# Kernel tuning notes

Measured on AMD Instinct MI355X. Metric: run time of the kernel, lower is better.

Reference implementation:

```python
import jax, jax.numpy as jnp
import numpy as np

D_MODEL = 1024
NUM_HEADS = 16
HEAD_DIM = D_MODEL // NUM_HEADS
T = 4096


def setup_inputs() -> dict:
    key = jax.random.key(0)
    x = jax.random.normal(key, (T, D_MODEL), dtype=jnp.float32)
    return {"x": x}


def reference(x) -> jnp.ndarray:
    T_, _ = x.shape
    # q = k = v = x reshaped to [heads, T, head_dim]
    qkv = x.reshape(T_, NUM_HEADS, HEAD_DIM).transpose(1, 0, 2)  # [H, T, hd]
    scale = 1.0 / (HEAD_DIM ** 0.5)
    scores = jnp.einsum('htd,hsd->hts', qkv, qkv) * scale  # [H, T, T]
    attn = jax.nn.softmax(scores, axis=-1)
    out = jnp.einsum('hts,hsd->htd', attn, qkv)  # [H, T, hd]
    return out.transpose(1, 0, 2).reshape(T_, D_MODEL)
```

## Files before the change

kernel.cpp:

```cpp
#include <hip/hip_runtime.h>
#include <hip/hip_bf16.h>

#define T_SEQ 4096
#define DMODEL 1024
#define NHEADS 16
#define HDIM 64
#define QBLK 256
#define SBLK 64
#define NTILES (T_SEQ / SBLK)
#define KSPLIT 2
#define TILES_PER_SPLIT (NTILES / KSPLIT)

#define KV_BYTES ((size_t)NHEADS * NTILES * 16384)
#define P_BYTES  ((size_t)KSPLIT * T_SEQ * DMODEL * 4)
#define L_BYTES  ((size_t)KSPLIT * NHEADS * T_SEQ * 4)
#define WS_NEEDED (KV_BYTES + P_BYTES + L_BYTES)

typedef __attribute__((ext_vector_type(8))) __bf16 bf16x8;
typedef __attribute__((ext_vector_type(4))) __bf16 bf16x4;
typedef __attribute__((ext_vector_type(16))) float f32x16;
typedef __attribute__((ext_vector_type(2))) unsigned uint32x2;

#define SWZ(row, col) ((col) ^ (((row) & 7) << 3))

#define QSCALE 0.1803368801111204f

__device__ __forceinline__ unsigned cvt_pk_bf16(float lo, float hi) {
  unsigned r;
  asm("v_cvt_pk_bf16_f32 %0, %1, %2" : "=v"(r) : "v"(lo), "v"(hi));
  return r;
}
__device__ __forceinline__ uint32x2 plswap(unsigned a, unsigned b) {
  return __builtin_amdgcn_permlane32_swap(a, b, false, false);
}
__device__ __forceinline__ float xhalf_max(float v) {
  uint32x2 r = plswap(__float_as_uint(v), __float_as_uint(v));
  return fmaxf(__uint_as_float(r[0]), __uint_as_float(r[1]));
}
__device__ __forceinline__ float xhalf_sum(float v) {
  uint32x2 r = plswap(__float_as_uint(v), __float_as_uint(v));
  return __uint_as_float(r[0]) + __uint_as_float(r[1]);
}
__device__ __forceinline__ void glds16(const void* g, void* l) {
  __builtin_amdgcn_global_load_lds(
      (const __attribute__((address_space(1))) unsigned int*)g,
      (__attribute__((address_space(3))) unsigned int*)l, 16, 0, 0);
}

__global__ __launch_bounds__(256) void prepass_kernel(
    const float* __restrict__ x, unsigned char* __restrict__ kvimg) {
  const int tid = threadIdx.x;
  const int c4 = tid & 15, s4 = tid >> 4;
  const int t = blockIdx.x & (NTILES - 1), h = blockIdx.x >> 6;
  const float* src = x + (size_t)(t * SBLK + s4 * 4) * DMODEL + h * HDIM + c4 * 4;
  float4 r0 = *reinterpret_cast<const float4*>(src);
  float4 r1 = *reinterpret_cast<const float4*>(src + DMODEL);
  float4 r2 = *reinterpret_cast<const float4*>(src + 2 * DMODEL);
  float4 r3 = *reinterpret_cast<const float4*>(src + 3 * DMODEL);
  __bf16 b[4][4];
  b[0][0] = (__bf16)r0.x; b[0][1] = (__bf16)r0.y; b[0][2] = (__bf16)r0.z; b[0][3] = (__bf16)r0.w;
  b[1][0] = (__bf16)r1.x; b[1][1] = (__bf16)r1.y; b[1][2] = (__bf16)r1.z; b[1][3] = (__bf16)r1.w;
  b[2][0] = (__bf16)r2.x; b[2][1] = (__bf16)r2.y; b[2][2] = (__bf16)r2.z; b[2][3] = (__bf16)r2.w;
  b[3][0] = (__bf16)r3.x; b[3][1] = (__bf16)r3.y; b[3][2] = (__bf16)r3.z; b[3][3] = (__bf16)r3.w;
  __bf16* Kimg = (__bf16*)(kvimg + (size_t)blockIdx.x * 16384);
  __bf16* Vimg = Kimg + 4096;
  #pragma unroll
  for (int j = 0; j < 4; j++) {
    const int s = s4 * 4 + j;
    bf16x4 kv; kv[0] = b[j][0]; kv[1] = b[j][1]; kv[2] = b[j][2]; kv[3] = b[j][3];
    *reinterpret_cast<bf16x4*>(&Kimg[s * 64 + SWZ(s, c4 * 4)]) = kv;
  }
  #pragma unroll
  for (int i = 0; i < 4; i++) {
    const int d = c4 * 4 + i;
    bf16x4 vv; vv[0] = b[0][i]; vv[1] = b[1][i]; vv[2] = b[2][i]; vv[3] = b[3][i];
    *reinterpret_cast<bf16x4*>(&Vimg[d * 64 + SWZ(d, s4 * 4)]) = vv;
  }
}

__global__ __launch_bounds__(256, 2) void attn_main_kernel(
    const float* __restrict__ x, const unsigned char* __restrict__ kvimg,
    float* __restrict__ pbuf, float* __restrict__ lbuf) {
  const int tid  = threadIdx.x;
  const int wave = tid >> 6;
  const int lane = tid & 63;
  const int lq   = lane & 31;
  const int hi   = lane >> 5;

  const int qt = blockIdx.x & 15;
  const int h  = blockIdx.x >> 4;
  const int sp = blockIdx.y;

  __shared__ __align__(16) unsigned char kvbytes[2][16384];

  bf16x8 qf[2][4];
  const int qrow0 = qt * QBLK + wave * 64 + lq;
  #pragma unroll
  for (int qs = 0; qs < 2; qs++) {
    const float* qp = x + (size_t)(qrow0 + qs * 32) * DMODEL + h * HDIM;
    #pragma unroll
    for (int ds = 0; ds < 4; ds++) {
      float4 a = *reinterpret_cast<const float4*>(qp + ds * 16 + hi * 8);
      float4 b = *reinterpret_cast<const float4*>(qp + ds * 16 + hi * 8 + 4);
      bf16x8 f;
      f[0] = (__bf16)(QSCALE * a.x); f[1] = (__bf16)(QSCALE * a.y);
      f[2] = (__bf16)(QSCALE * a.z); f[3] = (__bf16)(QSCALE * a.w);
      f[4] = (__bf16)(QSCALE * b.x); f[5] = (__bf16)(QSCALE * b.y);
      f[6] = (__bf16)(QSCALE * b.z); f[7] = (__bf16)(QSCALE * b.w);
      qf[qs][ds] = f;
    }
  }

  f32x16 oacc[2][2];
  float lsum[2];
  #pragma unroll
  for (int qs = 0; qs < 2; qs++) {
    #pragma unroll
    for (int dt = 0; dt < 2; dt++)
      #pragma unroll
      for (int r = 0; r < 16; r++) oacc[qs][dt][r] = 0.f;
    lsum[qs] = 0.f;
  }

  const unsigned char* tbase =
      kvimg + ((size_t)(h * NTILES + sp * TILES_PER_SPLIT) * 16384);

  auto STAGE = [&](int buf, int t) {
    const unsigned char* g = tbase + (size_t)t * 16384;
    #pragma unroll
    for (int i = 0; i < 4; i++)
      glds16(g + i * 4096 + tid * 16, &kvbytes[buf][i * 4096 + tid * 16]);
  };

  STAGE(0, 0);
  __syncthreads();
  int cur = 0;

  for (int t = 0; t < TILES_PER_SPLIT; t++) {
    if (t + 1 < TILES_PER_SPLIT) STAGE(cur ^ 1, t + 1);
    const __bf16 (*Kl)[64] = reinterpret_cast<const __bf16(*)[64]>(&kvbytes[cur][0]);
    const __bf16 (*Vt)[64] = reinterpret_cast<const __bf16(*)[64]>(&kvbytes[cur][8192]);

    f32x16 sacc[2][2];
    #pragma unroll
    for (int qs = 0; qs < 2; qs++)
      #pragma unroll
      for (int kt = 0; kt < 2; kt++)
        #pragma unroll
        for (int r = 0; r < 16; r++) sacc[qs][kt][r] = 0.f;
    #pragma unroll
    for (int kt = 0; kt < 2; kt++) {
      #pragma unroll
      for (int ds = 0; ds < 4; ds++) {
        bf16x8 kb = *reinterpret_cast<const bf16x8*>(
            &Kl[kt * 32 + lq][SWZ(lq, ds * 16 + hi * 8)]);
        #pragma unroll
        for (int qs = 0; qs < 2; qs++)
          sacc[qs][kt] = __builtin_amdgcn_mfma_f32_32x32x16_bf16(
              kb, qf[qs][ds], sacc[qs][kt], 0, 0, 0);
      }
    }

    #pragma unroll
    for (int qs = 0; qs < 2; qs++) {
      float rs = 0.f;
      #pragma unroll
      for (int kt = 0; kt < 2; kt++)
        #pragma unroll
        for (int r = 0; r < 16; r++) {
          float p = __builtin_amdgcn_exp2f(sacc[qs][kt][r]);
          sacc[qs][kt][r] = p;
          rs += p;
        }
      lsum[qs] += xhalf_sum(rs);
    }

    bf16x8 pf[2][4];
    #pragma unroll
    for (int qs = 0; qs < 2; qs++) {
      #pragma unroll
      for (int kt = 0; kt < 2; kt++) {
        #pragma unroll
        for (int b2 = 0; b2 < 2; b2++) {
          const int base = 8 * b2;
          unsigned dA0 = cvt_pk_bf16(sacc[qs][kt][base + 0], sacc[qs][kt][base + 1]);
          unsigned dA1 = cvt_pk_bf16(sacc[qs][kt][base + 2], sacc[qs][kt][base + 3]);
          unsigned dB0 = cvt_pk_bf16(sacc[qs][kt][base + 4], sacc[qs][kt][base + 5]);
          unsigned dB1 = cvt_pk_bf16(sacc[qs][kt][base + 6], sacc[qs][kt][base + 7]);
          uint32x2 r0 = plswap(dA0, dB0);
          uint32x2 r1 = plswap(dA1, dB1);
          uint4 u; u.x = r0[0]; u.y = r1[0]; u.z = r0[1]; u.w = r1[1];
          pf[qs][kt * 2 + b2] = *reinterpret_cast<bf16x8*>(&u);
        }
      }
    }

    #pragma unroll
    for (int dt = 0; dt < 2; dt++) {
      #pragma unroll
      for (int ks = 0; ks < 4; ks++) {
        bf16x8 vb = *reinterpret_cast<const bf16x8*>(
            &Vt[dt * 32 + lq][SWZ(lq, ks * 16 + hi * 8)]);
        #pragma unroll
        for (int qs = 0; qs < 2; qs++)
          oacc[qs][dt] = __builtin_amdgcn_mfma_f32_32x32x16_bf16(
              vb, pf[qs][ks], oacc[qs][dt], 0, 0, 0);
      }
    }

    __syncthreads();
    cur ^= 1;
  }

  #pragma unroll
  for (int qs = 0; qs < 2; qs++) {
    const int qrow = qrow0 + qs * 32;
    float* prow = pbuf + (size_t)sp * T_SEQ * DMODEL +
                  (size_t)qrow * DMODEL + h * HDIM;
    #pragma unroll
    for (int dt = 0; dt < 2; dt++) {
      #pragma unroll
      for (int m = 0; m < 4; m++) {
        float4 o;
        o.x = oacc[qs][dt][4 * m + 0]; o.y = oacc[qs][dt][4 * m + 1];
        o.z = oacc[qs][dt][4 * m + 2]; o.w = oacc[qs][dt][4 * m + 3];
        *reinterpret_cast<float4*>(&prow[dt * 32 + 8 * m + 4 * hi]) = o;
      }
    }
    if (hi == 0)
      lbuf[(size_t)(sp * NHEADS + h) * T_SEQ + qrow] = lsum[qs];
  }
}

__global__ __launch_bounds__(256) void merge_kernel(
    const float* __restrict__ pbuf, const float* __restrict__ lbuf,
    float* __restrict__ out) {
  const int gid = blockIdx.x * 256 + threadIdx.x;
  const int row = gid >> 8;
  const int h = (gid & 255) >> 4;
  const float l0 = lbuf[(size_t)h * T_SEQ + row];
  const float l1 = lbuf[(size_t)(NHEADS + h) * T_SEQ + row];
  const float invL = 1.f / (l0 + l1);
  const float4 p0 = reinterpret_cast<const float4*>(pbuf)[gid];
  const float4 p1 = reinterpret_cast<const float4*>(pbuf)[(size_t)T_SEQ * DMODEL / 4 + gid];
  float4 o;
  o.x = (p0.x + p1.x) * invL;
  o.y = (p0.y + p1.y) * invL;
  o.z = (p0.z + p1.z) * invL;
  o.w = (p0.w + p1.w) * invL;
  reinterpret_cast<float4*>(out)[gid] = o;
}

__global__ __launch_bounds__(256) void attn_fallback_kernel(
    const float* __restrict__ x, float* __restrict__ out) {
  const int tid  = threadIdx.x;
  const int wave = tid >> 6;
  const int lane = tid & 63;
  const int lq   = lane & 31;
  const int hi   = lane >> 5;
  const int qt = blockIdx.x & 31;
  const int h  = blockIdx.x >> 5;
  __shared__ __bf16 Kl[SBLK][HDIM];
  __shared__ __bf16 Vt[HDIM][SBLK];
  bf16x8 qf[4];
  const int qrow = qt * 128 + wave * 32 + lq;
  {
    const float* qp = x + (size_t)qrow * DMODEL + h * HDIM;
    #pragma unroll
    for (int ds = 0; ds < 4; ds++) {
      float4 a = *reinterpret_cast<const float4*>(qp + ds * 16 + hi * 8);
      float4 b = *reinterpret_cast<const float4*>(qp + ds * 16 + hi * 8 + 4);
      bf16x8 f;
      f[0] = (__bf16)(QSCALE * a.x); f[1] = (__bf16)(QSCALE * a.y);
      f[2] = (__bf16)(QSCALE * a.z); f[3] = (__bf16)(QSCALE * a.w);
      f[4] = (__bf16)(QSCALE * b.x); f[5] = (__bf16)(QSCALE * b.y);
      f[6] = (__bf16)(QSCALE * b.z); f[7] = (__bf16)(QSCALE * b.w);
      qf[ds] = f;
    }
  }
  float m_run = -1e30f, l_run = 0.f;
  f32x16 oacc[2];
  #pragma unroll
  for (int dt = 0; dt < 2; dt++)
    #pragma unroll
    for (int r = 0; r < 16; r++) oacc[dt][r] = 0.f;
  const float* xh = x + h * HDIM;
  const int c4 = tid & 15;
  const int s4 = tid >> 4;
  for (int t0 = 0; t0 < T_SEQ; t0 += SBLK) {
    __syncthreads();
    {
      const float* src = xh + (size_t)(t0 + s4 * 4) * DMODEL + c4 * 4;
      float4 r0 = *reinterpret_cast<const float4*>(src);
      float4 r1 = *reinterpret_cast<const float4*>(src + DMODEL);
      float4 r2 = *reinterpret_cast<const float4*>(src + 2 * DMODEL);
      float4 r3 = *reinterpret_cast<const float4*>(src + 3 * DMODEL);
      __bf16 b[4][4];
      b[0][0] = (__bf16)r0.x; b[0][1] = (__bf16)r0.y; b[0][2] = (__bf16)r0.z; b[0][3] = (__bf16)r0.w;
      b[1][0] = (__bf16)r1.x; b[1][1] = (__bf16)r1.y; b[1][2] = (__bf16)r1.z; b[1][3] = (__bf16)r1.w;
      b[2][0] = (__bf16)r2.x; b[2][1] = (__bf16)r2.y; b[2][2] = (__bf16)r2.z; b[2][3] = (__bf16)r2.w;
      b[3][0] = (__bf16)r3.x; b[3][1] = (__bf16)r3.y; b[3][2] = (__bf16)r3.z; b[3][3] = (__bf16)r3.w;
      #pragma unroll
      for (int j = 0; j < 4; j++) {
        const int s = s4 * 4 + j;
        bf16x4 kv; kv[0] = b[j][0]; kv[1] = b[j][1]; kv[2] = b[j][2]; kv[3] = b[j][3];
        *reinterpret_cast<bf16x4*>(&Kl[s][SWZ(s, c4 * 4)]) = kv;
      }
      #pragma unroll
      for (int i = 0; i < 4; i++) {
        const int d = c4 * 4 + i;
        bf16x4 vv; vv[0] = b[0][i]; vv[1] = b[1][i]; vv[2] = b[2][i]; vv[3] = b[3][i];
        *reinterpret_cast<bf16x4*>(&Vt[d][SWZ(d, s4 * 4)]) = vv;
      }
    }
    __syncthreads();
    f32x16 sacc[2];
    #pragma unroll
    for (int kt = 0; kt < 2; kt++)
      #pragma unroll
      for (int r = 0; r < 16; r++) sacc[kt][r] = 0.f;
    #pragma unroll
    for (int kt = 0; kt < 2; kt++) {
      #pragma unroll
      for (int ds = 0; ds < 4; ds++) {
        bf16x8 kb = *reinterpret_cast<const bf16x8*>(
            &Kl[kt * 32 + lq][SWZ(lq, ds * 16 + hi * 8)]);
        sacc[kt] = __builtin_amdgcn_mfma_f32_32x32x16_bf16(
            kb, qf[ds], sacc[kt], 0, 0, 0);
      }
    }
    float mx = sacc[0][0];
    #pragma unroll
    for (int kt = 0; kt < 2; kt++)
      #pragma unroll
      for (int r = 0; r < 16; r++) mx = fmaxf(mx, sacc[kt][r]);
    mx = xhalf_max(mx);
    const float mn = fmaxf(m_run, mx);
    const float corr = __builtin_amdgcn_exp2f(m_run - mn);
    #pragma unroll
    for (int dt = 0; dt < 2; dt++)
      #pragma unroll
      for (int r = 0; r < 16; r++) oacc[dt][r] *= corr;
    l_run *= corr;
    m_run = mn;
    float rs = 0.f;
    #pragma unroll
    for (int kt = 0; kt < 2; kt++)
      #pragma unroll
      for (int r = 0; r < 16; r++) {
        float p = __builtin_amdgcn_exp2f(sacc[kt][r] - mn);
        sacc[kt][r] = p;
        rs += p;
      }
    l_run += xhalf_sum(rs);
    bf16x8 pf[4];
    #pragma unroll
    for (int kt = 0; kt < 2; kt++) {
      #pragma unroll
      for (int b2 = 0; b2 < 2; b2++) {
        const int base = 8 * b2;
        unsigned dA0 = cvt_pk_bf16(sacc[kt][base + 0], sacc[kt][base + 1]);
        unsigned dA1 = cvt_pk_bf16(sacc[kt][base + 2], sacc[kt][base + 3]);
        unsigned dB0 = cvt_pk_bf16(sacc[kt][base + 4], sacc[kt][base + 5]);
        unsigned dB1 = cvt_pk_bf16(sacc[kt][base + 6], sacc[kt][base + 7]);
        uint32x2 r0 = plswap(dA0, dB0);
        uint32x2 r1 = plswap(dA1, dB1);
        uint4 u; u.x = r0[0]; u.y = r1[0]; u.z = r0[1]; u.w = r1[1];
        pf[kt * 2 + b2] = *reinterpret_cast<bf16x8*>(&u);
      }
    }
    #pragma unroll
    for (int dt = 0; dt < 2; dt++) {
      #pragma unroll
      for (int ks = 0; ks < 4; ks++) {
        bf16x8 vb = *reinterpret_cast<const bf16x8*>(
            &Vt[dt * 32 + lq][SWZ(lq, ks * 16 + hi * 8)]);
        oacc[dt] = __builtin_amdgcn_mfma_f32_32x32x16_bf16(
            vb, pf[ks], oacc[dt], 0, 0, 0);
      }
    }
  }
  const float inv = 1.f / l_run;
  float* orow = out + (size_t)qrow * DMODEL + h * HDIM;
  #pragma unroll
  for (int dt = 0; dt < 2; dt++) {
    #pragma unroll
    for (int m = 0; m < 4; m++) {
      float4 o;
      o.x = oacc[dt][4 * m + 0] * inv; o.y = oacc[dt][4 * m + 1] * inv;
      o.z = oacc[dt][4 * m + 2] * inv; o.w = oacc[dt][4 * m + 3] * inv;
      *reinterpret_cast<float4*>(&orow[dt * 32 + 8 * m + 4 * hi]) = o;
    }
  }
}

extern "C" void kernel_launch(void* const* d_in, const int* in_sizes, int n_in,
                              void* d_out, int out_size, void* d_ws, size_t ws_size,
                              hipStream_t stream) {
  const float* x = (const float*)d_in[0];
  float* out = (float*)d_out;
  if (ws_size >= WS_NEEDED) {
    unsigned char* kvimg = (unsigned char*)d_ws;
    float* pbuf = (float*)(kvimg + KV_BYTES);
    float* lbuf = (float*)(kvimg + KV_BYTES + P_BYTES);
    prepass_kernel<<<NHEADS * NTILES, 256, 0, stream>>>(x, kvimg);
    dim3 grid(NHEADS * (T_SEQ / QBLK), KSPLIT);
    attn_main_kernel<<<grid, 256, 0, stream>>>(x, kvimg, pbuf, lbuf);
    merge_kernel<<<T_SEQ * DMODEL / 4 / 256, 256, 0, stream>>>(pbuf, lbuf, out);
  } else {
    attn_fallback_kernel<<<NHEADS * (T_SEQ / 128), 256, 0, stream>>>(x, out);
  }
}
```

Before: 148.8 us.

## Software-pipeline QK of next tile with softmax/PV using triple-buffered LDS

```diff
diff --git a/kernel.cpp b/kernel.cpp
--- a/kernel.cpp
+++ b/kernel.cpp
@@ -5,11 +5,11 @@
 #define DMODEL 1024
 #define NHEADS 16
 #define HDIM 64
-#define QBLK 256
+#define QBLK 128
 #define SBLK 64
 #define NTILES (T_SEQ / SBLK)
 #define KSPLIT 2
-#define TILES_PER_SPLIT (NTILES / KSPLIT)
+#define NT (NTILES / KSPLIT)
 
 #define KV_BYTES ((size_t)NHEADS * NTILES * 16384)
 #define P_BYTES  ((size_t)KSPLIT * T_SEQ * DMODEL * 4)
@@ -87,17 +87,16 @@
   const int lq   = lane & 31;
   const int hi   = lane >> 5;
 
-  const int qt = blockIdx.x & 15;
-  const int h  = blockIdx.x >> 4;
+  const int qt = blockIdx.x & 31;
+  const int h  = blockIdx.x >> 5;
   const int sp = blockIdx.y;
 
-  __shared__ __align__(16) unsigned char kvbytes[2][16384];
-
-  bf16x8 qf[2][4];
-  const int qrow0 = qt * QBLK + wave * 64 + lq;
-  #pragma unroll
-  for (int qs = 0; qs < 2; qs++) {
-    const float* qp = x + (size_t)(qrow0 + qs * 32) * DMODEL + h * HDIM;
+  __shared__ __align__(16) unsigned char kvbytes[3][16384];
+
+  bf16x8 qf[4];
+  const int qrow = qt * QBLK + wave * 32 + lq;
+  {
+    const float* qp = x + (size_t)qrow * DMODEL + h * HDIM;
     #pragma unroll
     for (int ds = 0; ds < 4; ds++) {
       float4 a = *reinterpret_cast<const float4*>(qp + ds * 16 + hi * 8);
@@ -107,23 +106,19 @@
       f[2] = (__bf16)(QSCALE * a.z); f[3] = (__bf16)(QSCALE * a.w);
       f[4] = (__bf16)(QSCALE * b.x); f[5] = (__bf16)(QSCALE * b.y);
       f[6] = (__bf16)(QSCALE * b.z); f[7] = (__bf16)(QSCALE * b.w);
-      qf[qs][ds] = f;
-    }
-  }
-
-  f32x16 oacc[2][2];
-  float lsum[2];
-  #pragma unroll
-  for (int qs = 0; qs < 2; qs++) {
-    #pragma unroll
-    for (int dt = 0; dt < 2; dt++)
-      #pragma unroll
-      for (int r = 0; r < 16; r++) oacc[qs][dt][r] = 0.f;
-    lsum[qs] = 0.f;
-  }
+      qf[ds] = f;
+    }
+  }
+
+  f32x16 oacc[2];
+  float lsum = 0.f;
+  #pragma unroll
+  for (int dt = 0; dt < 2; dt++)
+    #pragma unroll
+    for (int r = 0; r < 16; r++) oacc[dt][r] = 0.f;
 
   const unsigned char* tbase =
-      kvimg + ((size_t)(h * NTILES + sp * TILES_PER_SPLIT) * 16384);
+      kvimg + ((size_t)(h * NTILES + sp * NT) * 16384);
 
   auto STAGE = [&](int buf, int t) {
     const unsigned char* g = tbase + (size_t)t * 16384;
@@ -132,104 +127,90 @@
       glds16(g + i * 4096 + tid * 16, &kvbytes[buf][i * 4096 + tid * 16]);
   };
 
-  STAGE(0, 0);
-  __syncthreads();
-  int cur = 0;
-
-  for (int t = 0; t < TILES_PER_SPLIT; t++) {
-    if (t + 1 < TILES_PER_SPLIT) STAGE(cur ^ 1, t + 1);
-    const __bf16 (*Kl)[64] = reinterpret_cast<const __bf16(*)[64]>(&kvbytes[cur][0]);
-    const __bf16 (*Vt)[64] = reinterpret_cast<const __bf16(*)[64]>(&kvbytes[cur][8192]);
-
-    f32x16 sacc[2][2];
-    #pragma unroll
-    for (int qs = 0; qs < 2; qs++)
-      #pragma unroll
-      for (int kt = 0; kt < 2; kt++)
-        #pragma unroll
-        for (int r = 0; r < 16; r++) sacc[qs][kt][r] = 0.f;
+  auto QK = [&](int buf, f32x16 (&s)[2]) {
+    const __bf16 (*Kl)[64] = reinterpret_cast<const __bf16(*)[64]>(&kvbytes[buf][0]);
     #pragma unroll
     for (int kt = 0; kt < 2; kt++) {
+      #pragma unroll
+      for (int r = 0; r < 16; r++) s[kt][r] = 0.f;
       #pragma unroll
       for (int ds = 0; ds < 4; ds++) {
         bf16x8 kb = *reinterpret_cast<const bf16x8*>(
             &Kl[kt * 32 + lq][SWZ(lq, ds * 16 + hi * 8)]);
-        #pragma unroll
-        for (int qs = 0; qs < 2; qs++)
-          sacc[qs][kt] = __builtin_amdgcn_mfma_f32_32x32x16_bf16(
-              kb, qf[qs][ds], sacc[qs][kt], 0, 0, 0);
-      }
-    }
-
-    #pragma unroll
-    for (int qs = 0; qs < 2; qs++) {
-      float rs = 0.f;
-      #pragma unroll
-      for (int kt = 0; kt < 2; kt++)
-        #pragma unroll
-        for (int r = 0; r < 16; r++) {
-          float p = __builtin_amdgcn_exp2f(sacc[qs][kt][r]);
-          sacc[qs][kt][r] = p;
-          rs += p;
-        }
-      lsum[qs] += xhalf_sum(rs);
-    }
-
-    bf16x8 pf[2][4];
-    #pragma unroll
-    for (int qs = 0; qs < 2; qs++) {
-      #pragma unroll
-      for (int kt = 0; kt < 2; kt++) {
-        #pragma unroll
-        for (int b2 = 0; b2 < 2; b2++) {
-          const int base = 8 * b2;
-          unsigned dA0 = cvt_pk_bf16(sacc[qs][kt][base + 0], sacc[qs][kt][base + 1]);
-          unsigned dA1 = cvt_pk_bf16(sacc[qs][kt][base + 2], sacc[qs][kt][base + 3]);
-          unsigned dB0 = cvt_pk_bf16(sacc[qs][kt][base + 4], sacc[qs][kt][base + 5]);
-          unsigned dB1 = cvt_pk_bf16(sacc[qs][kt][base + 6], sacc[qs][kt][base + 7]);
-          uint32x2 r0 = plswap(dA0, dB0);
-          uint32x2 r1 = plswap(dA1, dB1);
-          uint4 u; u.x = r0[0]; u.y = r1[0]; u.z = r0[1]; u.w = r1[1];
-          pf[qs][kt * 2 + b2] = *reinterpret_cast<bf16x8*>(&u);
-        }
-      }
-    }
-
+        s[kt] = __builtin_amdgcn_mfma_f32_32x32x16_bf16(kb, qf[ds], s[kt], 0, 0, 0);
+      }
+    }
+  };
+
+  auto BODY = [&](int t, f32x16 (&scur)[2], f32x16 (&snext)[2]) {
+    const int bc = t % 3, bn = (t + 1) % 3, bs = (t + 2) % 3;
+    if (t + 1 < NT) QK(bn, snext);
+    if (t + 2 < NT) STAGE(bs, t + 2);
+    float rs = 0.f;
+    #pragma unroll
+    for (int kt = 0; kt < 2; kt++)
+      #pragma unroll
+      for (int r = 0; r < 16; r++) {
+        float p = __builtin_amdgcn_exp2f(scur[kt][r]);
+        scur[kt][r] = p;
+        rs += p;
+      }
+    lsum += xhalf_sum(rs);
+    bf16x8 pf[4];
+    #pragma unroll
+    for (int kt = 0; kt < 2; kt++) {
+      #pragma unroll
+      for (int b2 = 0; b2 < 2; b2++) {
+        const int base = 8 * b2;
+        unsigned dA0 = cvt_pk_bf16(scur[kt][base + 0], scur[kt][base + 1]);
+        unsigned dA1 = cvt_pk_bf16(scur[kt][base + 2], scur[kt][base + 3]);
+        unsigned dB0 = cvt_pk_bf16(scur[kt][base + 4], scur[kt][base + 5]);
+        unsigned dB1 = cvt_pk_bf16(scur[kt][base + 6], scur[kt][base + 7]);
+        uint32x2 r0 = plswap(dA0, dB0);
+        uint32x2 r1 = plswap(dA1, dB1);
+        uint4 u; u.x = r0[0]; u.y = r1[0]; u.z = r0[1]; u.w = r1[1];
+        pf[kt * 2 + b2] = *reinterpret_cast<bf16x8*>(&u);
+      }
+    }
+    const __bf16 (*Vt)[64] = reinterpret_cast<const __bf16(*)[64]>(&kvbytes[bc][8192]);
     #pragma unroll
     for (int dt = 0; dt < 2; dt++) {
       #pragma unroll
       for (int ks = 0; ks < 4; ks++) {
         bf16x8 vb = *reinterpret_cast<const bf16x8*>(
             &Vt[dt * 32 + lq][SWZ(lq, ks * 16 + hi * 8)]);
-        #pragma unroll
-        for (int qs = 0; qs < 2; qs++)
-          oacc[qs][dt] = __builtin_amdgcn_mfma_f32_32x32x16_bf16(
-              vb, pf[qs][ks], oacc[qs][dt], 0, 0, 0);
-      }
-    }
-
+        oacc[dt] = __builtin_amdgcn_mfma_f32_32x32x16_bf16(vb, pf[ks], oacc[dt], 0, 0, 0);
+      }
+    }
     __syncthreads();
-    cur ^= 1;
-  }
-
-  #pragma unroll
-  for (int qs = 0; qs < 2; qs++) {
-    const int qrow = qrow0 + qs * 32;
-    float* prow = pbuf + (size_t)sp * T_SEQ * DMODEL +
-                  (size_t)qrow * DMODEL + h * HDIM;
-    #pragma unroll
-    for (int dt = 0; dt < 2; dt++) {
-      #pragma unroll
-      for (int m = 0; m < 4; m++) {
-        float4 o;
-        o.x = oacc[qs][dt][4 * m + 0]; o.y = oacc[qs][dt][4 * m + 1];
-        o.z = oacc[qs][dt][4 * m + 2]; o.w = oacc[qs][dt][4 * m + 3];
-        *reinterpret_cast<float4*>(&prow[dt * 32 + 8 * m + 4 * hi]) = o;
-      }
-    }
-    if (hi == 0)
-      lbuf[(size_t)(sp * NHEADS + h) * T_SEQ + qrow] = lsum[qs];
-  }
+  };
+
+  f32x16 sA[2], sB[2];
+  STAGE(0, 0);
+  __syncthreads();
+  STAGE(1, 1);
+  QK(0, sA);
+  __syncthreads();
+
+  for (int t = 0; t < NT; t += 2) {
+    BODY(t, sA, sB);
+    BODY(t + 1, sB, sA);
+  }
+
+  float* prow = pbuf + (size_t)sp * T_SEQ * DMODEL +
+                (size_t)qrow * DMODEL + h * HDIM;
+  #pragma unroll
+  for (int dt = 0; dt < 2; dt++) {
+    #pragma unroll
+    for (int m = 0; m < 4; m++) {
+      float4 o;
+      o.x = oacc[dt][4 * m + 0]; o.y = oacc[dt][4 * m + 1];
+      o.z = oacc[dt][4 * m + 2]; o.w = oacc[dt][4 * m + 3];
+      *reinterpret_cast<float4*>(&prow[dt * 32 + 8 * m + 4 * hi]) = o;
+    }
+  }
+  if (hi == 0)
+    lbuf[(size_t)(sp * NHEADS + h) * T_SEQ + qrow] = lsum;
 }
 
 __global__ __launch_bounds__(256) void merge_kernel(
```

New measurement: 155.6 us. 4.5% more time.
